# Kernel tuning notes

Hardware: AMD Instinct MI355X
Metric: run time of the kernel (lower is better)

## Reference

```python
import jax, jax.numpy as jnp
import numpy as np
from jax import lax

EPS = 1e-5  # torch BatchNorm2d default


def setup_inputs() -> dict:
    key = jax.random.key(0)
    k1, k2, k3 = jax.random.split(key, 3)
    C = 64
    x = jax.random.normal(k1, (32, C, 128, 128), dtype=jnp.float32)
    # per-channel 3x3 depthwise weights (OIHW with I=1, feature_group_count=C)
    w = jax.random.normal(k2, (C, 1, 3, 3), dtype=jnp.float32) * (1.0 / 3.0)
    b = jax.random.normal(k3, (C,), dtype=jnp.float32) * 0.1
    gamma = jnp.ones((C,), dtype=jnp.float32)
    beta = jnp.zeros((C,), dtype=jnp.float32)
    return {"x": x, "w": w, "b": b, "gamma": gamma, "beta": beta}


def reference(x, w, b, gamma, beta):
    C = x.shape[1]
    # depthwise 3x3 conv, stride 1, padding 1 (same math as C separate Conv2d(1,1,3))
    y = lax.conv_general_dilated(
        x, w,
        window_strides=(1, 1),
        padding=((1, 1), (1, 1)),
        feature_group_count=C,
        dimension_numbers=("NCHW", "OIHW", "NCHW"),
    )
    y = y + b[None, :, None, None]
    # BatchNorm2d(1) per channel in training mode: batch stats over (N, H, W),
    # biased variance, eps=1e-5
    mean = jnp.mean(y, axis=(0, 2, 3), keepdims=True)
    var = jnp.var(y, axis=(0, 2, 3), keepdims=True)
    y_hat = (y - mean) * lax.rsqrt(var + EPS)
    out = y_hat * gamma[None, :, None, None] + beta[None, :, None, None]
    return jax.nn.relu(out)
```

## Files before the change

### kernel.cpp

```cpp
#include <hip/hip_runtime.h>

#define HW        128
#define PLANE     (HW * HW)
#define NCH       64
#define NB        32
#define NPLANES   (NB * NCH)
#define HALF_ROWS 64
#define LDS_ROWS  66
#define LDS_STR   136
#define COUNT_INV (1.0f / 524288.0f)
#define EPSV      1e-5f


__device__ __forceinline__ void stage_halfplane(const float* __restrict__ x,
                                                int plane, int half, float* ld) {
    const int t = threadIdx.x;
    for (int i = t; i < LDS_ROWS * LDS_STR; i += 256) ld[i] = 0.f;
    __syncthreads();
    const float4* xp = (const float4*)(x + (size_t)plane * PLANE);
    const int h0base = half * HALF_ROWS;
    for (int f = t; f < LDS_ROWS * 32; f += 256) {
        int r  = f >> 5;
        int c4 = f & 31;
        int g  = h0base - 1 + r;
        if ((unsigned)g < (unsigned)HW) {
            float4 v = xp[g * 32 + c4];
            *(float4*)&ld[r * LDS_STR + 4 + c4 * 4] = v;
        }
    }
    __syncthreads();
}

__device__ __forceinline__ void conv4(const float* ld, int h0l, int wcol,
                                      const float* W, float bias, float acc[4]) {
    float v[6][3];
#pragma unroll
    for (int i = 0; i < 6; ++i)
#pragma unroll
        for (int j = 0; j < 3; ++j)
            v[i][j] = ld[(h0l + i) * LDS_STR + wcol + 3 + j];
#pragma unroll
    for (int k = 0; k < 4; ++k) {
        float a = bias;
#pragma unroll
        for (int kh = 0; kh < 3; ++kh)
#pragma unroll
            for (int kw = 0; kw < 3; ++kw)
                a = fmaf(v[k + kh][kw], W[kh * 3 + kw], a);
        acc[k] = a;
    }
}

__global__ __launch_bounds__(256) void dwconv_reduce(const float* __restrict__ x,
                                                     const float* __restrict__ wgt,
                                                     const float* __restrict__ bias,
                                                     float* __restrict__ partials) {
    __shared__ float ld[LDS_ROWS * LDS_STR];
    __shared__ float red[8];
    const int bid   = blockIdx.x;
    const int plane = bid >> 1;
    const int half  = bid & 1;
    const int c     = plane & 63;
    const int t     = threadIdx.x;

    float W[9];
#pragma unroll
    for (int k = 0; k < 9; ++k) W[k] = wgt[c * 9 + k];
    const float bv = bias[c];

    stage_halfplane(x, plane, half, ld);

    const int wcol = t & 127;
    const int trow = t >> 7;
    float sum = 0.f, sq = 0.f;
#pragma unroll
    for (int jj = 0; jj < 8; ++jj) {
        int h0l = (trow + jj * 2) * 4;
        float acc[4];
        conv4(ld, h0l, wcol, W, bv, acc);
#pragma unroll
        for (int k = 0; k < 4; ++k) {
            sum += acc[k];
            sq   = fmaf(acc[k], acc[k], sq);
        }
    }
#pragma unroll
    for (int off = 32; off; off >>= 1) {
        sum += __shfl_down(sum, off);
        sq  += __shfl_down(sq, off);
    }
    const int wave = t >> 6, lane = t & 63;
    if (lane == 0) { red[wave] = sum; red[4 + wave] = sq; }
    __syncthreads();
    if (t == 0) {
        float S = red[0] + red[1] + red[2] + red[3];
        float Q = red[4] + red[5] + red[6] + red[7];
        partials[bid]        = S;
        partials[8192 + bid] = Q;
    }
}

__global__ void bn_stats(const float* __restrict__ partials,
                         const float* __restrict__ gamma,
                         const float* __restrict__ beta,
                         float* __restrict__ st) {
    int c = threadIdx.x;
    if (c < NCH) {
        float S = 0.f, Q = 0.f;
        for (int n = 0; n < NB; ++n) {
            int base = (n * NCH + c) * 2;
            S += partials[base] + partials[base + 1];
            Q += partials[8192 + base] + partials[8192 + base + 1];
        }
        float mean = S * COUNT_INV;
        float var  = fmaxf(Q * COUNT_INV - mean * mean, 0.f);
        float s    = gamma[c] * rsqrtf(var + EPSV);
        st[c]        = s;
        st[NCH + c]  = beta[c] - mean * s;
    }
}

__global__ __launch_bounds__(256) void dwconv_apply(const float* __restrict__ x,
                                                    const float* __restrict__ wgt,
                                                    const float* __restrict__ bias,
                                                    const float* __restrict__ st,
                                                    float* __restrict__ out) {
    __shared__ float ld[LDS_ROWS * LDS_STR];
    const int bid   = blockIdx.x;
    const int plane = bid >> 1;
    const int half  = bid & 1;
    const int c     = plane & 63;
    const int t     = threadIdx.x;

    float W[9];
#pragma unroll
    for (int k = 0; k < 9; ++k) W[k] = wgt[c * 9 + k];
    const float bv = bias[c];
    const float s  = st[c];
    const float sh = st[NCH + c];

    stage_halfplane(x, plane, half, ld);

    const int wcol = t & 127;
    const int trow = t >> 7;
    float* op = out + (size_t)plane * PLANE + (size_t)(half * HALF_ROWS) * HW;
#pragma unroll
    for (int jj = 0; jj < 8; ++jj) {
        int h0l = (trow + jj * 2) * 4;
        float acc[4];
        conv4(ld, h0l, wcol, W, bv, acc);
#pragma unroll
        for (int k = 0; k < 4; ++k) {
            float r = fmaf(acc[k], s, sh);
            op[(h0l + k) * HW + wcol] = fmaxf(r, 0.f);
        }
    }
}

extern "C" void kernel_launch(void* const* d_in, const int* in_sizes, int n_in,
                              void* d_out, int out_size, void* d_ws, size_t ws_size,
                              hipStream_t stream) {
    const float* x     = (const float*)d_in[0];
    const float* w     = (const float*)d_in[1];
    const float* b     = (const float*)d_in[2];
    const float* gamma = (const float*)d_in[3];
    const float* beta  = (const float*)d_in[4];
    float* out = (float*)d_out;
    float* ws  = (float*)d_ws;

    dwconv_reduce<<<NPLANES * 2, 256, 0, stream>>>(x, w, b, ws);
    bn_stats<<<1, 64, 0, stream>>>(ws, gamma, beta, ws + 16384);
    dwconv_apply<<<NPLANES * 2, 256, 0, stream>>>(x, w, b, ws + 16384, out);
}
```

Before: 86.72 us.

## Replace LDS staging with register sliding-window conv and fold BN stats into apply

Both passes drop the shared-memory staging of a half-plane and instead have each thread load float4 rows plus halo scalars straight from global memory, keeping a 3-row register window as it walks 16 rows. Each block now covers a full plane, with float4 stores in the apply pass. The separate bn_stats kernel is removed: every apply block reduces the 32 per-batch partials for its channel itself, which saves one launch and the LDS barriers at the cost of redundant small reductions and unaligned halo loads.

```diff
diff --git a/kernel.cpp b/kernel.cpp
--- a/kernel.cpp
+++ b/kernel.cpp
@@ -1,89 +1,81 @@
 #include <hip/hip_runtime.h>
 
 #define HW        128
-#define PLANE     (HW * HW)
+#define PLANE     16384
 #define NCH       64
 #define NB        32
-#define NPLANES   (NB * NCH)
-#define HALF_ROWS 64
-#define LDS_ROWS  66
-#define LDS_STR   136
+#define NPLANES   2048
 #define COUNT_INV (1.0f / 524288.0f)
 #define EPSV      1e-5f
 
 
-__device__ __forceinline__ void stage_halfplane(const float* __restrict__ x,
-                                                int plane, int half, float* ld) {
-    const int t = threadIdx.x;
-    for (int i = t; i < LDS_ROWS * LDS_STR; i += 256) ld[i] = 0.f;
-    __syncthreads();
-    const float4* xp = (const float4*)(x + (size_t)plane * PLANE);
-    const int h0base = half * HALF_ROWS;
-    for (int f = t; f < LDS_ROWS * 32; f += 256) {
-        int r  = f >> 5;
-        int c4 = f & 31;
-        int g  = h0base - 1 + r;
-        if ((unsigned)g < (unsigned)HW) {
-            float4 v = xp[g * 32 + c4];
-            *(float4*)&ld[r * LDS_STR + 4 + c4 * 4] = v;
-        }
-    }
-    __syncthreads();
-}
-
-__device__ __forceinline__ void conv4(const float* ld, int h0l, int wcol,
-                                      const float* W, float bias, float acc[4]) {
-    float v[6][3];
-#pragma unroll
-    for (int i = 0; i < 6; ++i)
-#pragma unroll
-        for (int j = 0; j < 3; ++j)
-            v[i][j] = ld[(h0l + i) * LDS_STR + wcol + 3 + j];
-#pragma unroll
-    for (int k = 0; k < 4; ++k) {
-        float a = bias;
-#pragma unroll
-        for (int kh = 0; kh < 3; ++kh)
-#pragma unroll
-            for (int kw = 0; kw < 3; ++kw)
-                a = fmaf(v[k + kh][kw], W[kh * 3 + kw], a);
-        acc[k] = a;
+__device__ __forceinline__ void load_row(const float* __restrict__ bp, int g, int w4,
+                                         bool hasL, bool hasR, float (&v)[6]) {
+    if ((unsigned)g < (unsigned)HW) {
+        const float* rp = bp + g * HW + w4;
+        float4 m = *(const float4*)rp;
+        v[0] = hasL ? rp[-1] : 0.f;
+        v[1] = m.x; v[2] = m.y; v[3] = m.z; v[4] = m.w;
+        v[5] = hasR ? rp[4] : 0.f;
+    } else {
+        v[0] = 0.f; v[1] = 0.f; v[2] = 0.f; v[3] = 0.f; v[4] = 0.f; v[5] = 0.f;
     }
 }
 
-__global__ __launch_bounds__(256) void dwconv_reduce(const float* __restrict__ x,
+__device__ __forceinline__ void conv_row(const float (&tp)[6], const float (&md)[6],
+                                         const float (&bt)[6], const float* W,
+                                         float bias, float (&acc)[4]) {
+#pragma unroll
+    for (int j = 0; j < 4; ++j) {
+        float a = bias;
+        a = fmaf(tp[j],     W[0], a);
+        a = fmaf(tp[j + 1], W[1], a);
+        a = fmaf(tp[j + 2], W[2], a);
+        a = fmaf(md[j],     W[3], a);
+        a = fmaf(md[j + 1], W[4], a);
+        a = fmaf(md[j + 2], W[5], a);
+        a = fmaf(bt[j],     W[6], a);
+        a = fmaf(bt[j + 1], W[7], a);
+        a = fmaf(bt[j + 2], W[8], a);
+        acc[j] = a;
+    }
+}
+
+__global__ __launch_bounds__(256, 4) void pass_stats(const float* __restrict__ x,
                                                      const float* __restrict__ wgt,
                                                      const float* __restrict__ bias,
                                                      float* __restrict__ partials) {
-    __shared__ float ld[LDS_ROWS * LDS_STR];
     __shared__ float red[8];
-    const int bid   = blockIdx.x;
-    const int plane = bid >> 1;
-    const int half  = bid & 1;
-    const int c     = plane & 63;
-    const int t     = threadIdx.x;
+    const int p  = blockIdx.x;
+    const int c  = p & 63;
+    const int t  = threadIdx.x;
+    const int cg = t & 31, rg = t >> 5;
+    const int w4 = cg * 4, r0 = rg * 16;
 
     float W[9];
 #pragma unroll
     for (int k = 0; k < 9; ++k) W[k] = wgt[c * 9 + k];
     const float bv = bias[c];
+    const float* bp = x + (size_t)p * PLANE;
+    const bool hasL = (cg != 0), hasR = (cg != 31);
 
-    stage_halfplane(x, plane, half, ld);
+    float v[3][6];
+    load_row(bp, r0 - 1, w4, hasL, hasR, v[0]);
+    load_row(bp, r0,     w4, hasL, hasR, v[1]);
 
-    const int wcol = t & 127;
-    const int trow = t >> 7;
     float sum = 0.f, sq = 0.f;
 #pragma unroll
-    for (int jj = 0; jj < 8; ++jj) {
-        int h0l = (trow + jj * 2) * 4;
+    for (int i = 0; i < 16; ++i) {
+        load_row(bp, r0 + 1 + i, w4, hasL, hasR, v[(i + 2) % 3]);
         float acc[4];
-        conv4(ld, h0l, wcol, W, bv, acc);
+        conv_row(v[i % 3], v[(i + 1) % 3], v[(i + 2) % 3], W, bv, acc);
 #pragma unroll
-        for (int k = 0; k < 4; ++k) {
-            sum += acc[k];
-            sq   = fmaf(acc[k], acc[k], sq);
+        for (int j = 0; j < 4; ++j) {
+            sum += acc[j];
+            sq = fmaf(acc[j], acc[j], sq);
         }
     }
+
 #pragma unroll
     for (int off = 32; off; off >>= 1) {
         sum += __shfl_down(sum, off);
@@ -93,67 +85,69 @@
     if (lane == 0) { red[wave] = sum; red[4 + wave] = sq; }
     __syncthreads();
     if (t == 0) {
-        float S = red[0] + red[1] + red[2] + red[3];
-        float Q = red[4] + red[5] + red[6] + red[7];
-        partials[bid]        = S;
-        partials[8192 + bid] = Q;
+        partials[p]           = red[0] + red[1] + red[2] + red[3];
+        partials[NPLANES + p] = red[4] + red[5] + red[6] + red[7];
     }
 }
 
-__global__ void bn_stats(const float* __restrict__ partials,
-                         const float* __restrict__ gamma,
-                         const float* __restrict__ beta,
-                         float* __restrict__ st) {
-    int c = threadIdx.x;
-    if (c < NCH) {
-        float S = 0.f, Q = 0.f;
-        for (int n = 0; n < NB; ++n) {
-            int base = (n * NCH + c) * 2;
-            S += partials[base] + partials[base + 1];
-            Q += partials[8192 + base] + partials[8192 + base + 1];
+__global__ __launch_bounds__(256, 4) void pass_apply(const float* __restrict__ x,
+                                                     const float* __restrict__ wgt,
+                                                     const float* __restrict__ bias,
+                                                     const float* __restrict__ partials,
+                                                     const float* __restrict__ gamma,
+                                                     const float* __restrict__ beta,
+                                                     float* __restrict__ out) {
+    __shared__ float ssh[2];
+    const int p  = blockIdx.x;
+    const int c  = p & 63;
+    const int t  = threadIdx.x;
+    const int cg = t & 31, rg = t >> 5;
+    const int w4 = cg * 4, r0 = rg * 16;
+
+    if (t < 32) {
+        float S = partials[t * NCH + c];
+        float Q = partials[NPLANES + t * NCH + c];
+#pragma unroll
+        for (int off = 16; off; off >>= 1) {
+            S += __shfl_down(S, off);
+            Q += __shfl_down(Q, off);
         }
-        float mean = S * COUNT_INV;
-        float var  = fmaxf(Q * COUNT_INV - mean * mean, 0.f);
-        float s    = gamma[c] * rsqrtf(var + EPSV);
-        st[c]        = s;
-        st[NCH + c]  = beta[c] - mean * s;
+        if (t == 0) {
+            float mean = S * COUNT_INV;
+            float var  = fmaxf(Q * COUNT_INV - mean * mean, 0.f);
+            float s    = gamma[c] * rsqrtf(var + EPSV);
+            ssh[0] = s;
+            ssh[1] = beta[c] - mean * s;
+        }
     }
-}
-
-__global__ __launch_bounds__(256) void dwconv_apply(const float* __restrict__ x,
-                                                    const float* __restrict__ wgt,
-                                                    const float* __restrict__ bias,
-                                                    const float* __restrict__ st,
-                                                    float* __restrict__ out) {
-    __shared__ float ld[LDS_ROWS * LDS_STR];
-    const int bid   = blockIdx.x;
-    const int plane = bid >> 1;
-    const int half  = bid & 1;
-    const int c     = plane & 63;
-    const int t     = threadIdx.x;
 
     float W[9];
 #pragma unroll
     for (int k = 0; k < 9; ++k) W[k] = wgt[c * 9 + k];
     const float bv = bias[c];
-    const float s  = st[c];
-    const float sh = st[NCH + c];
+    __syncthreads();
+    const float s  = ssh[0];
+    const float sh = fmaf(bv, s, ssh[1]);
 
-    stage_halfplane(x, plane, half, ld);
+    const float* bp = x + (size_t)p * PLANE;
+    float* op = out + (size_t)p * PLANE;
+    const bool hasL = (cg != 0), hasR = (cg != 31);
 
-    const int wcol = t & 127;
-    const int trow = t >> 7;
-    float* op = out + (size_t)plane * PLANE + (size_t)(half * HALF_ROWS) * HW;
+    float v[3][6];
+    load_row(bp, r0 - 1, w4, hasL, hasR, v[0]);
+    load_row(bp, r0,     w4, hasL, hasR, v[1]);
+
 #pragma unroll
-    for (int jj = 0; jj < 8; ++jj) {
-        int h0l = (trow + jj * 2) * 4;
+    for (int i = 0; i < 16; ++i) {
+        load_row(bp, r0 + 1 + i, w4, hasL, hasR, v[(i + 2) % 3]);
         float acc[4];
-        conv4(ld, h0l, wcol, W, bv, acc);
-#pragma unroll
-        for (int k = 0; k < 4; ++k) {
-            float r = fmaf(acc[k], s, sh);
-            op[(h0l + k) * HW + wcol] = fmaxf(r, 0.f);
-        }
+        conv_row(v[i % 3], v[(i + 1) % 3], v[(i + 2) % 3], W, 0.f, acc);
+        float4 o;
+        o.x = fmaxf(fmaf(acc[0], s, sh), 0.f);
+        o.y = fmaxf(fmaf(acc[1], s, sh), 0.f);
+        o.z = fmaxf(fmaf(acc[2], s, sh), 0.f);
+        o.w = fmaxf(fmaf(acc[3], s, sh), 0.f);
+        *(float4*)(op + (r0 + i) * HW + w4) = o;
     }
 }
 
@@ -168,7 +162,6 @@
     float* out = (float*)d_out;
     float* ws  = (float*)d_ws;
 
-    dwconv_reduce<<<NPLANES * 2, 256, 0, stream>>>(x, w, b, ws);
-    bn_stats<<<1, 64, 0, stream>>>(ws, gamma, beta, ws + 16384);
-    dwconv_apply<<<NPLANES * 2, 256, 0, stream>>>(x, w, b, ws + 16384, out);
+    pass_stats<<<NPLANES, 256, 0, stream>>>(x, w, b, ws);
+    pass_apply<<<NPLANES, 256, 0, stream>>>(x, w, b, ws, gamma, beta, out);
 }
```

Result: faster. 79.17 us (-8.7%).
